# Kernel tuning notes

Measured on AMD Instinct MI355X. Metric: run time of the kernel, lower is better.

The kernel has to match this reference:

```python
import jax, jax.numpy as jnp
import numpy as np

HEADS = 4
CH = 64  # hidden_channels (per-head out channels)
N_INT = 50000
N_LANE = 400000
E_PO = 400000
E_ADJ = 200000


def setup_inputs() -> dict:
    key = jax.random.key(0)
    ks = iter(jax.random.split(key, 32))
    rn = lambda shape, s=0.1: jax.random.normal(next(ks), shape, dtype=jnp.float32) * s
    inp = {
        'x_int': rn((N_INT, 16), 1.0),
        'x_lane': rn((N_LANE, 12), 1.0),
        'h0': jnp.zeros((N_INT, CH), jnp.float32),
        'enc_int_W': rn((16, CH)), 'enc_int_b': jnp.zeros((CH,), jnp.float32),
        'enc_lane_W': rn((12, CH)), 'enc_lane_b': jnp.zeros((CH,), jnp.float32),
        'Wsrc_po': rn((CH, HEADS * CH)), 'Wdst_po': rn((CH, HEADS * CH)),
        'att_src_po': rn((HEADS, CH)), 'att_dst_po': rn((HEADS, CH)),
        'bias_po': jnp.zeros((HEADS * CH,), jnp.float32),
        'Wsrc_adj': rn((CH, HEADS * CH)), 'Wdst_adj': rn((CH, HEADS * CH)),
        'att_src_adj': rn((HEADS, CH)), 'att_dst_adj': rn((HEADS, CH)),
        'bias_adj': jnp.zeros((HEADS * CH,), jnp.float32),
        'gru_W_ih': rn((3 * CH, HEADS * CH)), 'gru_W_hh': rn((3 * CH, CH)),
        'gru_b_ih': jnp.zeros((3 * CH,), jnp.float32), 'gru_b_hh': jnp.zeros((3 * CH,), jnp.float32),
        'W_pi': rn((CH, 8)), 'b_pi': jnp.zeros((8,), jnp.float32),
        'W_v': rn((CH, 1)), 'b_v': jnp.zeros((1,), jnp.float32),
        'src_po': jax.random.randint(next(ks), (E_PO,), 0, N_LANE),
        'dst_po': jax.random.randint(next(ks), (E_PO,), 0, N_INT),
        'src_adj': jax.random.randint(next(ks), (E_ADJ,), 0, N_INT),
        'dst_adj': jax.random.randint(next(ks), (E_ADJ,), 0, N_INT),
    }
    return inp


def gat_conv(x_src, x_dst, src, dst, Wsrc, Wdst, a_src, a_dst, bias, n_dst):
    # PyG GATConv (bipartite, concat=True, no self loops), negative_slope=0.2
    hs = (x_src @ Wsrc).reshape(-1, HEADS, CH)  # [Ns,H,C]
    hd = (x_dst @ Wdst).reshape(-1, HEADS, CH)  # [Nd,H,C]
    a_s = jnp.einsum('nhc,hc->nh', hs, a_src)   # [Ns,H]
    a_d = jnp.einsum('nhc,hc->nh', hd, a_dst)   # [Nd,H]
    alpha = jax.nn.leaky_relu(a_s[src] + a_d[dst], 0.2)        # [E,H]
    amax = jax.ops.segment_max(alpha, dst, num_segments=n_dst)  # [Nd,H]
    ex = jnp.exp(alpha - amax[dst])
    den = jax.ops.segment_sum(ex, dst, num_segments=n_dst)
    w = ex / den[dst]                                           # [E,H] softmax per dst
    msg = hs[src] * w[:, :, None]                               # [E,H,C]
    out = jax.ops.segment_sum(msg, dst, num_segments=n_dst)     # [Nd,H,C]
    return out.reshape(n_dst, HEADS * CH) + bias


def gru_cell(x, h, W_ih, W_hh, b_ih, b_hh):
    gi = x @ W_ih.T + b_ih
    gh = h @ W_hh.T + b_hh
    i_r, i_z, i_n = jnp.split(gi, 3, axis=1)
    h_r, h_z, h_n = jnp.split(gh, 3, axis=1)
    r = jax.nn.sigmoid(i_r + h_r)
    z = jax.nn.sigmoid(i_z + h_z)
    n = jnp.tanh(i_n + r * h_n)
    return (1.0 - z) * n + z * h


def reference(x_int, x_lane, h0, enc_int_W, enc_int_b, enc_lane_W, enc_lane_b,
              Wsrc_po, Wdst_po, att_src_po, att_dst_po, bias_po,
              Wsrc_adj, Wdst_adj, att_src_adj, att_dst_adj, bias_adj,
              gru_W_ih, gru_W_hh, gru_b_ih, gru_b_hh,
              W_pi, b_pi, W_v, b_v,
              src_po, dst_po, src_adj, dst_adj):
    # per-type encoders + ReLU
    e_int = jax.nn.relu(x_int @ enc_int_W + enc_int_b)    # [N_int,CH]
    e_lane = jax.nn.relu(x_lane @ enc_lane_W + enc_lane_b)  # [N_lane,CH]
    # HeteroConv aggr='sum' over relations targeting 'intersection'
    o_po = gat_conv(e_lane, e_int, src_po, dst_po, Wsrc_po, Wdst_po,
                    att_src_po, att_dst_po, bias_po, N_INT)
    o_adj = gat_conv(e_int, e_int, src_adj, dst_adj, Wsrc_adj, Wdst_adj,
                     att_src_adj, att_dst_adj, bias_adj, N_INT)
    inter = jax.nn.relu(o_po + o_adj)  # dropout = identity (deterministic eval)
    h_new = gru_cell(inter, h0, gru_W_ih, gru_W_hh, gru_b_ih, gru_b_hh)
    logits = h_new @ W_pi + b_pi
    value = h_new @ W_v + b_v
    return logits, value, h_new
```

## Files before the change

kernel.cpp:

```cpp
#include <hip/hip_runtime.h>

#define NI 50000
#define NL 400000
#define EPO 400000
#define EADJ 200000

#define K1_ITER 8
#define K2_ITER 4
#define K1_ROWS (32*K1_ITER)
#define K2_ROWS (32*K2_ITER)
#define NLB ((NL + K1_ROWS - 1)/K1_ROWS)
#define NIB ((NI + K2_ROWS - 1)/K2_ROWS)
#define NHB ((EPO + EADJ + 255)/256)

typedef unsigned int u32;
typedef unsigned short u16;
typedef short bf16x8 __attribute__((ext_vector_type(8)));
typedef float f32x4 __attribute__((ext_vector_type(4)));

__device__ __forceinline__ float bf2f(u16 h){ return __uint_as_float(((u32)h)<<16); }
__device__ __forceinline__ u16 f2bf(float f){
  u32 u = __float_as_uint(f);
  u += 0x7FFFu + ((u>>16)&1u);
  return (u16)(u>>16);
}
__device__ __forceinline__ u32 pack2(float a, float b){
  return (u32)f2bf(a) | ((u32)f2bf(b)<<16);
}

__device__ __forceinline__ float b2_val(
    const float* __restrict__ W_ih, const float* __restrict__ W_hh, int m, int k)
{
  if(k < 256){ return (m<192) ? W_ih[m*256+k] : 0.f; }
  int kk = k-256;
  if(m<128) return W_hh[m*64+kk];
  if(m>=192) return W_hh[(m-64)*64+kk];
  return 0.f;
}

__global__ __launch_bounds__(256) void k0_prep(
    const float* __restrict__ Wsrc_po, const float* __restrict__ att_src_po,
    const float* __restrict__ Wdst_po, const float* __restrict__ att_dst_po,
    const float* __restrict__ Wsrc_adj, const float* __restrict__ att_src_adj,
    const float* __restrict__ Wdst_adj, const float* __restrict__ att_dst_adj,
    const float* __restrict__ W_ih, const float* __restrict__ W_hh,
    const float* __restrict__ bias_po, const float* __restrict__ bias_adj,
    const float* __restrict__ b_ih, const float* __restrict__ b_hh,
    float* __restrict__ v4, u16* __restrict__ WheadT, u16* __restrict__ B2F,
    float* __restrict__ bias_comb, float* __restrict__ bias2,
    int* __restrict__ cnt)
{
  const int T0 = 1024, T1 = 4*64*128, T2 = 10*16*64*8;
  const int TC = 2*NI;
  int total = T0 + T1 + T2 + 256 + 256 + TC;
  for(int t = blockIdx.x*256 + threadIdx.x; t < total; t += gridDim.x*256){
    if(t < T0){
      int which = t>>8, hc = t&255, h = hc>>6, c = hc&63;
      const float *W, *att;
      if(which==0){ W=Wsrc_po;  att=att_src_po; }
      else if(which==1){ W=Wdst_po;  att=att_dst_po; }
      else if(which==2){ W=Wsrc_adj; att=att_src_adj; }
      else { W=Wdst_adj; att=att_dst_adj; }
      float s=0.f;
      for(int j=0;j<64;j++) s += W[c*256 + h*64 + j]*att[h*64+j];
      v4[which*256 + hc] = s;
    } else if(t < T0 + T1){
      int i = t - T0; int h = i>>13, rem = i&8191, m = rem>>7, k = rem&127;
      float val = (k<64) ? Wsrc_po[k*256 + h*64 + m]
                         : Wsrc_adj[(k-64)*256 + h*64 + m];
      WheadT[i] = f2bf(val);
    } else if(t < T0 + T1 + T2){
      int i = t - (T0+T1);
      int j = i&7;
      int u4 = i>>3;
      int kstep = u4>>10, rem = u4&1023, tile = rem>>6, lane = rem&63;
      int col = tile*16 + (lane&15);
      int k = kstep*32 + (lane>>4)*8 + j;
      B2F[i] = f2bf(b2_val(W_ih, W_hh, col, k));
    } else if(t < T0 + T1 + T2 + 256){
      int m = t - (T0+T1+T2);
      bias_comb[m] = bias_po[m] + bias_adj[m];
    } else if(t < T0 + T1 + T2 + 512){
      int m = t - (T0+T1+T2+256);
      float v;
      if(m<128) v = b_ih[m] + b_hh[m];
      else if(m<192) v = b_ih[m];
      else v = b_hh[m-64];
      bias2[m] = v;
    } else {
      cnt[t - (T0+T1+T2+512)] = 0;
    }
  }
}

__global__ __launch_bounds__(256) void k_enc(
    const float* __restrict__ x_lane, const float* __restrict__ Wl, const float* __restrict__ bl,
    const float* __restrict__ x_int,  const float* __restrict__ Wi, const float* __restrict__ bi,
    const float* __restrict__ v_sp, const float* __restrict__ v_dp,
    const float* __restrict__ v_sa, const float* __restrict__ v_da,
    u16* __restrict__ e_lane, float* __restrict__ a_s_po,
    u16* __restrict__ e_int, float* __restrict__ a_dp, float* __restrict__ a_sa,
    float* __restrict__ a_da,
    const int* __restrict__ dst_po, const int* __restrict__ dst_adj,
    int* __restrict__ cnt)
{
  int t = threadIdx.x;
  int wv = t>>6, l = t&63;
  int g = l&7, m = l>>3;
  int blk = blockIdx.x;
  if(blk < NLB){
    float wreg[12][8], breg[8];
#pragma unroll
    for(int k=0;k<12;k++){
      float4 w0 = *(const float4*)(Wl + k*64 + g*8);
      float4 w1 = *(const float4*)(Wl + k*64 + g*8 + 4);
      wreg[k][0]=w0.x; wreg[k][1]=w0.y; wreg[k][2]=w0.z; wreg[k][3]=w0.w;
      wreg[k][4]=w1.x; wreg[k][5]=w1.y; wreg[k][6]=w1.z; wreg[k][7]=w1.w;
    }
    {
      float4 b0 = *(const float4*)(bl + g*8);
      float4 b1 = *(const float4*)(bl + g*8 + 4);
      breg[0]=b0.x; breg[1]=b0.y; breg[2]=b0.z; breg[3]=b0.w;
      breg[4]=b1.x; breg[5]=b1.y; breg[6]=b1.z; breg[7]=b1.w;
    }
    int rowbase = blk*K1_ROWS + wv*(8*K1_ITER) + m;
    float4 Aa={0,0,0,0}, Ab={0,0,0,0}, Ac={0,0,0,0};
    float4 Ba={0,0,0,0}, Bb={0,0,0,0}, Bc={0,0,0,0};
    if(rowbase < NL){
      const float4* xp = (const float4*)(x_lane + (size_t)rowbase*12);
      Aa = xp[0]; Ab = xp[1]; Ac = xp[2];
    }
    if(rowbase+8 < NL){
      const float4* xp = (const float4*)(x_lane + (size_t)(rowbase+8)*12);
      Ba = xp[0]; Bb = xp[1]; Bc = xp[2];
    }
#pragma unroll
    for(int it=0; it<K1_ITER; it++){
      int row = rowbase + it*8;
      float4 Ca={0,0,0,0}, Cb={0,0,0,0}, Cc={0,0,0,0};
      if(it+2 < K1_ITER && row+16 < NL){
        const float4* xp = (const float4*)(x_lane + (size_t)(row+16)*12);
        Ca = xp[0]; Cb = xp[1]; Cc = xp[2];
      }
      float xv[12];
      xv[0]=Aa.x; xv[1]=Aa.y; xv[2]=Aa.z; xv[3]=Aa.w;
      xv[4]=Ab.x; xv[5]=Ab.y; xv[6]=Ab.z; xv[7]=Ab.w;
      xv[8]=Ac.x; xv[9]=Ac.y; xv[10]=Ac.z; xv[11]=Ac.w;
      float acc[8];
#pragma unroll
      for(int j=0;j<8;j++) acc[j]=breg[j];
#pragma unroll
      for(int k=0;k<12;k++){
        float xk = xv[k];
#pragma unroll
        for(int j=0;j<8;j++) acc[j] += xk*wreg[k][j];
      }
      float e[8];
#pragma unroll
      for(int j=0;j<8;j++) e[j] = fmaxf(acc[j], 0.f);
      float as[4];
#pragma unroll
      for(int h=0;h<4;h++){
        float4 v0 = *(const float4*)(v_sp + h*64 + g*8);
        float4 v1 = *(const float4*)(v_sp + h*64 + g*8 + 4);
        as[h] = e[0]*v0.x + e[1]*v0.y + e[2]*v0.z + e[3]*v0.w
              + e[4]*v1.x + e[5]*v1.y + e[6]*v1.z + e[7]*v1.w;
      }
#pragma unroll
      for(int o=1;o<8;o<<=1){
#pragma unroll
        for(int h=0;h<4;h++) as[h] += __shfl_xor(as[h], o, 64);
      }
      if(row < NL){
        uint4 P;
        P.x = pack2(e[0],e[1]); P.y = pack2(e[2],e[3]);
        P.z = pack2(e[4],e[5]); P.w = pack2(e[6],e[7]);
        ((uint4*)e_lane)[(size_t)row*8 + g] = P;
        if(g==0){
          float4 A; A.x=as[0]; A.y=as[1]; A.z=as[2]; A.w=as[3];
          *(float4*)(a_s_po + (size_t)row*4) = A;
        }
      }
      Aa=Ba; Ab=Bb; Ac=Bc;
      Ba=Ca; Bb=Cb; Bc=Cc;
    }
  } else if(blk < NLB + NIB){
    int b2 = blk - NLB;
    float breg[8];
    {
      float4 b0 = *(const float4*)(bi + g*8);
      float4 b1 = *(const float4*)(bi + g*8 + 4);
      breg[0]=b0.x; breg[1]=b0.y; breg[2]=b0.z; breg[3]=b0.w;
      breg[4]=b1.x; breg[5]=b1.y; breg[6]=b1.z; breg[7]=b1.w;
    }
    int rowbase = b2*K2_ROWS + wv*(8*K2_ITER) + m;
#pragma unroll
    for(int it=0; it<K2_ITER; it++){
      int row = rowbase + it*8;
      float xv[16];
      if(row < NI){
        const float4* xp = (const float4*)(x_int + (size_t)row*16);
#pragma unroll
        for(int q=0;q<4;q++){
          float4 xq = xp[q];
          xv[q*4]=xq.x; xv[q*4+1]=xq.y; xv[q*4+2]=xq.z; xv[q*4+3]=xq.w;
        }
      } else {
#pragma unroll
        for(int k=0;k<16;k++) xv[k]=0.f;
      }
      float acc[8];
#pragma unroll
      for(int j=0;j<8;j++) acc[j]=breg[j];
#pragma unroll
      for(int k=0;k<16;k++){
        float4 w0 = *(const float4*)(Wi + k*64 + g*8);
        float4 w1 = *(const float4*)(Wi + k*64 + g*8 + 4);
        float xk = xv[k];
        acc[0] += xk*w0.x; acc[1] += xk*w0.y; acc[2] += xk*w0.z; acc[3] += xk*w0.w;
        acc[4] += xk*w1.x; acc[5] += xk*w1.y; acc[6] += xk*w1.z; acc[7] += xk*w1.w;
      }
      float e[8];
#pragma unroll
      for(int j=0;j<8;j++) e[j] = fmaxf(acc[j], 0.f);
      float ad[4], sa[4], da[4];
#pragma unroll
      for(int h=0;h<4;h++){
        float4 v0, v1;
        v0 = *(const float4*)(v_dp + h*64 + g*8); v1 = *(const float4*)(v_dp + h*64 + g*8 + 4);
        ad[h] = e[0]*v0.x + e[1]*v0.y + e[2]*v0.z + e[3]*v0.w
              + e[4]*v1.x + e[5]*v1.y + e[6]*v1.z + e[7]*v1.w;
        v0 = *(const float4*)(v_sa + h*64 + g*8); v1 = *(const float4*)(v_sa + h*64 + g*8 + 4);
        sa[h] = e[0]*v0.x + e[1]*v0.y + e[2]*v0.z + e[3]*v0.w
              + e[4]*v1.x + e[5]*v1.y + e[6]*v1.z + e[7]*v1.w;
        v0 = *(const float4*)(v_da + h*64 + g*8); v1 = *(const float4*)(v_da + h*64 + g*8 + 4);
        da[h] = e[0]*v0.x + e[1]*v0.y + e[2]*v0.z + e[3]*v0.w
              + e[4]*v1.x + e[5]*v1.y + e[6]*v1.z + e[7]*v1.w;
      }
#pragma unroll
      for(int o=1;o<8;o<<=1){
#pragma unroll
        for(int h=0;h<4;h++){
          ad[h] += __shfl_xor(ad[h], o, 64);
          sa[h] += __shfl_xor(sa[h], o, 64);
          da[h] += __shfl_xor(da[h], o, 64);
        }
      }
      if(row < NI){
        uint4 P;
        P.x = pack2(e[0],e[1]); P.y = pack2(e[2],e[3]);
        P.z = pack2(e[4],e[5]); P.w = pack2(e[6],e[7]);
        ((uint4*)e_int)[(size_t)row*8 + g] = P;
        if(g==0){
          float4 A;
          A.x=ad[0]; A.y=ad[1]; A.z=ad[2]; A.w=ad[3]; *(float4*)(a_dp + (size_t)row*4) = A;
          A.x=sa[0]; A.y=sa[1]; A.z=sa[2]; A.w=sa[3]; *(float4*)(a_sa + (size_t)row*4) = A;
          A.x=da[0]; A.y=da[1]; A.z=da[2]; A.w=da[3]; *(float4*)(a_da + (size_t)row*4) = A;
        }
      }
    }
  } else {
    int i = (blk - NLB - NIB)*256 + t;
    if(i < EPO) atomicAdd(&cnt[dst_po[i]], 1);
    else if(i < EPO+EADJ) atomicAdd(&cnt[NI + dst_adj[i-EPO]], 1);
  }
}

__global__ __launch_bounds__(1024) void k4a_scan(
    const int* __restrict__ cnt, int* __restrict__ offA, int* __restrict__ bsum)
{
  __shared__ int s[1024];
  int y = blockIdx.y;
  int i = blockIdx.x*1024 + threadIdx.x;
  int v = (i<NI) ? cnt[y*NI+i] : 0;
  s[threadIdx.x]=v;
  __syncthreads();
  for(int o=1;o<1024;o<<=1){
    int t = (threadIdx.x>=o) ? s[threadIdx.x-o] : 0;
    __syncthreads();
    s[threadIdx.x] += t;
    __syncthreads();
  }
  if(i<NI) offA[y*NI+i] = s[threadIdx.x]-v;
  if(threadIdx.x==1023) bsum[y*64+blockIdx.x] = s[1023];
}

__global__ __launch_bounds__(128) void k4b_scanb(int* __restrict__ bsum)
{
  int y = threadIdx.x>>6, lane = threadIdx.x&63;
  int v = (lane<49) ? bsum[y*64+lane] : 0;
  int orig = v;
#pragma unroll
  for(int o=1;o<64;o<<=1){
    int t = __shfl_up(v,o,64);
    if(lane>=o) v += t;
  }
  if(lane<49) bsum[y*64+lane] = v-orig;
}

__global__ __launch_bounds__(1024) void k4c_add(
    int* __restrict__ offA, int* __restrict__ cur, const int* __restrict__ bsum)
{
  int y = blockIdx.y;
  int i = blockIdx.x*1024 + threadIdx.x;
  if(i<NI){
    int o = offA[y*NI+i] + bsum[y*64+blockIdx.x];
    offA[y*NI+i]=o;
    cur[y*NI+i]=o;
  }
}

__global__ __launch_bounds__(256) void k5_scatter(
    const int* __restrict__ src_po, const int* __restrict__ dst_po,
    const int* __restrict__ src_adj, const int* __restrict__ dst_adj,
    const float* __restrict__ a_s_po, const float* __restrict__ a_d_po,
    const float* __restrict__ a_s_adj, const float* __restrict__ a_d_adj,
    int* __restrict__ cur, int* __restrict__ csr_po, int* __restrict__ csr_adj,
    float* __restrict__ pw_po, float* __restrict__ pw_adj)
{
  int i = blockIdx.x*256 + threadIdx.x;
  if(i < EPO){
    int s = src_po[i];
    int d = dst_po[i];
    int p = atomicAdd(&cur[d],1);
    csr_po[p] = s;
    float4 as = *(const float4*)(a_s_po + (size_t)s*4);
    float4 ad = *(const float4*)(a_d_po + (size_t)d*4);
    float4 pv;
    float x;
    x = as.x+ad.x; pv.x = __expf(x>0.f?x:0.2f*x);
    x = as.y+ad.y; pv.y = __expf(x>0.f?x:0.2f*x);
    x = as.z+ad.z; pv.z = __expf(x>0.f?x:0.2f*x);
    x = as.w+ad.w; pv.w = __expf(x>0.f?x:0.2f*x);
    *(float4*)(pw_po + (size_t)p*4) = pv;
  } else if(i < EPO+EADJ){
    int e = i-EPO;
    int s = src_adj[e];
    int d = dst_adj[e];
    int p = atomicAdd(&cur[NI+d],1);
    csr_adj[p] = s;
    float4 as = *(const float4*)(a_s_adj + (size_t)s*4);
    float4 ad = *(const float4*)(a_d_adj + (size_t)d*4);
    float4 pv;
    float x;
    x = as.x+ad.x; pv.x = __expf(x>0.f?x:0.2f*x);
    x = as.y+ad.y; pv.y = __expf(x>0.f?x:0.2f*x);
    x = as.z+ad.z; pv.z = __expf(x>0.f?x:0.2f*x);
    x = as.w+ad.w; pv.w = __expf(x>0.f?x:0.2f*x);
    *(float4*)(pw_adj + (size_t)p*4) = pv;
  }
}

__device__ __forceinline__ void agg_rel(
    int beg, int n, int lane,
    const int* __restrict__ csr, const float* __restrict__ pw,
    const u16* __restrict__ emat, u16* __restrict__ aggrow)
{
  float l0=0,l1=0,l2=0,l3=0;
  float c0=0,c1=0,c2=0,c3=0;
  for(int base=0;base<n;base+=64){
    int m = n-base; if(m>64) m=64;
    int sv_ = (lane<m) ? csr[beg+base+lane] : 0;
    int t2=0;
    for(; t2+1<m; t2+=2){
      int s0 = __shfl(sv_, t2, 64);
      int s1 = __shfl(sv_, t2+1, 64);
      float4 p0 = *(const float4*)(pw + (size_t)(beg+base+t2)*4);
      float4 p1 = *(const float4*)(pw + (size_t)(beg+base+t2+1)*4);
      float e0 = bf2f(emat[(size_t)s0*64+lane]);
      float e1 = bf2f(emat[(size_t)s1*64+lane]);
      c0 += p0.x*e0; c1 += p0.y*e0; c2 += p0.z*e0; c3 += p0.w*e0;
      l0 += p0.x;    l1 += p0.y;    l2 += p0.z;    l3 += p0.w;
      c0 += p1.x*e1; c1 += p1.y*e1; c2 += p1.z*e1; c3 += p1.w*e1;
      l0 += p1.x;    l1 += p1.y;    l2 += p1.z;    l3 += p1.w;
    }
    if(t2<m){
      int s0 = __shfl(sv_, t2, 64);
      float4 p0 = *(const float4*)(pw + (size_t)(beg+base+t2)*4);
      float e0 = bf2f(emat[(size_t)s0*64+lane]);
      c0 += p0.x*e0; c1 += p0.y*e0; c2 += p0.z*e0; c3 += p0.w*e0;
      l0 += p0.x;    l1 += p0.y;    l2 += p0.z;    l3 += p0.w;
    }
  }
  aggrow[lane]       = f2bf(n>0 ? c0/l0 : 0.f);
  aggrow[64+lane]    = f2bf(n>0 ? c1/l1 : 0.f);
  aggrow[128+lane]   = f2bf(n>0 ? c2/l2 : 0.f);
  aggrow[192+lane]   = f2bf(n>0 ? c3/l3 : 0.f);
}

__global__ __launch_bounds__(512) void k6_agg(
    const int* __restrict__ off, const int* __restrict__ cnt,
    const int* __restrict__ csr_po, const int* __restrict__ csr_adj,
    const float* __restrict__ pw_po, const float* __restrict__ pw_adj,
    const u16* __restrict__ e_lane, const u16* __restrict__ e_int,
    u16* __restrict__ agg)
{
  int wave=threadIdx.x>>6, lane=threadIdx.x&63;
  int d = blockIdx.x*4 + (wave&3);
  if(d>=NI) return;
  if(wave < 4)
    agg_rel(off[d],    cnt[d],    lane, csr_po,  pw_po,  e_lane, agg + (size_t)d*512);
  else
    agg_rel(off[NI+d], cnt[NI+d], lane, csr_adj, pw_adj, e_int,  agg + (size_t)d*512 + 256);
}

__global__ __launch_bounds__(256) void gemm_head(
    const u16* __restrict__ agg, const u16* __restrict__ WheadT,
    const float* __restrict__ bias, u16* __restrict__ inter256)
{
  __shared__ u16 As[64][136];
  __shared__ u16 Bs[64][136];
  int t=threadIdx.x, wave=t>>6, lane=t&63;
  int h = blockIdx.y;
  int row0 = blockIdx.x*64;
  int r = lane&15, q = lane>>4;
  const uint4* Bsrc = (const uint4*)(WheadT + (size_t)h*8192);
#pragma unroll
  for(int it=0; it<4; it++){
    int idx = it*256 + t;
    int brow = idx>>4, u4 = idx&15;
    *(uint4*)&Bs[brow][u4*8] = Bsrc[idx];
    int grow = row0 + brow;
    uint4 v = {0,0,0,0};
    if(grow < NI){
      int co = (u4<8) ? (h*64 + u4*8) : (256 + h*64 + (u4-8)*8);
      v = *(const uint4*)(agg + (size_t)grow*512 + co);
    }
    *(uint4*)&As[brow][u4*8] = v;
  }
  __syncthreads();
  f32x4 acc0={0,0,0,0}, acc1={0,0,0,0}, acc2={0,0,0,0}, acc3={0,0,0,0};
#pragma unroll
  for(int ks=0; ks<4; ks++){
    bf16x8 af = *(const bf16x8*)&As[wave*16 + r][q*8 + ks*32];
    bf16x8 b0 = *(const bf16x8*)&Bs[ 0 + r][q*8 + ks*32];
    bf16x8 b1 = *(const bf16x8*)&Bs[16 + r][q*8 + ks*32];
    bf16x8 b2 = *(const bf16x8*)&Bs[32 + r][q*8 + ks*32];
    bf16x8 b3 = *(const bf16x8*)&Bs[48 + r][q*8 + ks*32];
    acc0 = __builtin_amdgcn_mfma_f32_16x16x32_bf16(af,b0,acc0,0,0,0);
    acc1 = __builtin_amdgcn_mfma_f32_16x16x32_bf16(af,b1,acc1,0,0,0);
    acc2 = __builtin_amdgcn_mfma_f32_16x16x32_bf16(af,b2,acc2,0,0,0);
    acc3 = __builtin_amdgcn_mfma_f32_16x16x32_bf16(af,b3,acc3,0,0,0);
  }
  int crow_base = row0 + wave*16 + q*4;
#pragma unroll
  for(int t2=0;t2<4;t2++){
    f32x4 a = (t2==0)?acc0 : (t2==1)?acc1 : (t2==2)?acc2 : acc3;
    int col = h*64 + t2*16 + r;
    float bcol = bias[col];
#pragma unroll
    for(int rr=0;rr<4;rr++){
      int row = crow_base + rr;
      if(row < NI)
        inter256[(size_t)row*256 + col] = f2bf(fmaxf(a[rr]+bcol, 0.f));
    }
  }
}

__global__ __launch_bounds__(256) void k9_gru(
    const u16* __restrict__ inter256, const uint4* __restrict__ B2F,
    const float* __restrict__ bias2, const float* __restrict__ h0,
    const float* __restrict__ Wpi, const float* __restrict__ bpi,
    const float* __restrict__ Wv, const float* __restrict__ bvp,
    float* __restrict__ out)
{
  int t=threadIdx.x, w=t>>6, lane=t&63;
  int r = lane&15, q = lane>>4;
  int row0 = blockIdx.x*64;
  int arow = row0 + w*16 + r;
  int arc = arow < NI ? arow : NI-1;
  const u16* Aptr = inter256 + (size_t)arc*256 + q*8;
  const float* h0r = h0 + (size_t)arc*64 + q*8;
  f32x4 acc[16];
#pragma unroll
  for(int i=0;i<16;i++) acc[i] = (f32x4){0,0,0,0};
#pragma unroll
  for(int ks=0; ks<10; ks++){
    bf16x8 af;
    if(ks < 8){
      af = *(const bf16x8*)(Aptr + ks*32);
    } else {
      const float* hp = h0r + (ks-8)*32;
      float4 f0 = *(const float4*)(hp);
      float4 f1 = *(const float4*)(hp+4);
      uint4 P;
      P.x = pack2(f0.x,f0.y); P.y = pack2(f0.z,f0.w);
      P.z = pack2(f1.x,f1.y); P.w = pack2(f1.z,f1.w);
      *(uint4*)&af = P;
    }
    const uint4* bp = B2F + ks*1024 + lane;
#pragma unroll
    for(int tt=0;tt<16;tt++){
      uint4 bu = bp[tt*64];
      bf16x8 bf; *(uint4*)&bf = bu;
      acc[tt] = __builtin_amdgcn_mfma_f32_16x16x32_bf16(af, bf, acc[tt], 0,0,0);
    }
  }
  float pk[4][8];
  float pv[4];
#pragma unroll
  for(int rr=0;rr<4;rr++){
    pv[rr]=0.f;
#pragma unroll
    for(int j=0;j<8;j++) pk[rr][j]=0.f;
  }
  int rbase = row0 + w*16 + q*4;
#pragma unroll
  for(int t2=0;t2<4;t2++){
    int c = t2*16 + r;
    float b0 = bias2[c], b1 = bias2[64+c], b2 = bias2[128+c], b3 = bias2[192+c];
    float wp[8];
#pragma unroll
    for(int j=0;j<8;j++) wp[j] = Wpi[c*8+j];
    float wv = Wv[c];
#pragma unroll
    for(int rr=0;rr<4;rr++){
      int row = rbase + rr;
      float g0 = acc[t2][rr]    + b0;
      float g1 = acc[t2+4][rr]  + b1;
      float g2 = acc[t2+8][rr]  + b2;
      float g3 = acc[t2+12][rr] + b3;
      float h0v = (row < NI) ? h0[(size_t)row*64 + c] : 0.f;
      float rg = 1.f/(1.f+__expf(-g0));
      float zg = 1.f/(1.f+__expf(-g1));
      float e2 = __expf(2.f*(g2 + rg*g3));
      float ng = 1.f - 2.f/(e2+1.f);
      float h = (1.f-zg)*ng + zg*h0v;
      if(row < NI) out[450000 + (size_t)row*64 + c] = h;
#pragma unroll
      for(int j=0;j<8;j++) pk[rr][j] += h*wp[j];
      pv[rr] += h*wv;
    }
  }
#pragma unroll
  for(int o=1;o<16;o<<=1){
#pragma unroll
    for(int rr=0;rr<4;rr++){
#pragma unroll
      for(int j=0;j<8;j++) pk[rr][j] += __shfl_xor(pk[rr][j], o, 64);
      pv[rr] += __shfl_xor(pv[rr], o, 64);
    }
  }
  if(r==0){
#pragma unroll
    for(int rr=0;rr<4;rr++){
      int row = rbase + rr;
      if(row < NI){
#pragma unroll
        for(int j=0;j<8;j++) out[(size_t)row*8 + j] = pk[rr][j] + bpi[j];
        out[400000 + row] = pv[rr] + bvp[0];
      }
    }
  }
}

extern "C" void kernel_launch(void* const* d_in, const int* in_sizes, int n_in,
                              void* d_out, int out_size, void* d_ws, size_t ws_size,
                              hipStream_t stream) {
  const float* x_int      = (const float*)d_in[0];
  const float* x_lane     = (const float*)d_in[1];
  const float* h0         = (const float*)d_in[2];
  const float* enc_int_W  = (const float*)d_in[3];
  const float* enc_int_b  = (const float*)d_in[4];
  const float* enc_lane_W = (const float*)d_in[5];
  const float* enc_lane_b = (const float*)d_in[6];
  const float* Wsrc_po    = (const float*)d_in[7];
  const float* Wdst_po    = (const float*)d_in[8];
  const float* att_src_po = (const float*)d_in[9];
  const float* att_dst_po = (const float*)d_in[10];
  const float* bias_po    = (const float*)d_in[11];
  const float* Wsrc_adj   = (const float*)d_in[12];
  const float* Wdst_adj   = (const float*)d_in[13];
  const float* att_src_adj= (const float*)d_in[14];
  const float* att_dst_adj= (const float*)d_in[15];
  const float* bias_adj   = (const float*)d_in[16];
  const float* gru_W_ih   = (const float*)d_in[17];
  const float* gru_W_hh   = (const float*)d_in[18];
  const float* gru_b_ih   = (const float*)d_in[19];
  const float* gru_b_hh   = (const float*)d_in[20];
  const float* W_pi       = (const float*)d_in[21];
  const float* b_pi       = (const float*)d_in[22];
  const float* W_v        = (const float*)d_in[23];
  const float* b_v        = (const float*)d_in[24];
  const int* src_po  = (const int*)d_in[25];
  const int* dst_po  = (const int*)d_in[26];
  const int* src_adj = (const int*)d_in[27];
  const int* dst_adj = (const int*)d_in[28];
  float* out = (float*)d_out;

  char* w = (char*)d_ws;
  size_t ofs = 0;
  auto alloc = [&](size_t bytes)->char*{
    char* p = w + ofs;
    ofs = (ofs + bytes + 255) & ~(size_t)255;
    return p;
  };
  u16*  e_lane   = (u16*)alloc((size_t)NL*64*2);
  u16*  e_int    = (u16*)alloc((size_t)NI*64*2);
  float* a_s_po  = (float*)alloc((size_t)NL*4*4);
  float* a_d_po  = (float*)alloc((size_t)NI*4*4);
  float* a_s_adj = (float*)alloc((size_t)NI*4*4);
  float* a_d_adj = (float*)alloc((size_t)NI*4*4);
  int*  cnt      = (int*)alloc((size_t)2*NI*4);
  int*  offA     = (int*)alloc((size_t)2*NI*4);
  int*  cur      = (int*)alloc((size_t)2*NI*4);
  int*  csr_po   = (int*)alloc((size_t)EPO*4);
  int*  csr_adj  = (int*)alloc((size_t)EADJ*4);
  float* pw_po   = (float*)alloc((size_t)EPO*4*4);
  float* pw_adj  = (float*)alloc((size_t)EADJ*4*4);
  int*  bsum     = (int*)alloc(2*64*4);
  u16*  agg      = (u16*)alloc((size_t)NI*512*2);
  u16*  inter256 = (u16*)alloc((size_t)NI*256*2);
  u16*  WheadT   = (u16*)alloc(4*64*128*2);
  u16*  B2F      = (u16*)alloc(10*16*64*8*2);
  float* v4      = (float*)alloc(4*256*4);
  float* bias_comb = (float*)alloc(256*4);
  float* bias2   = (float*)alloc(256*4);
  (void)ws_size; (void)n_in; (void)in_sizes; (void)out_size;

  k0_prep<<<256, 256, 0, stream>>>(
      Wsrc_po, att_src_po, Wdst_po, att_dst_po,
      Wsrc_adj, att_src_adj, Wdst_adj, att_dst_adj,
      gru_W_ih, gru_W_hh, bias_po, bias_adj, gru_b_ih, gru_b_hh,
      v4, WheadT, B2F, bias_comb, bias2, cnt);
  k_enc<<<NLB+NIB+NHB, 256, 0, stream>>>(
      x_lane, enc_lane_W, enc_lane_b,
      x_int, enc_int_W, enc_int_b,
      v4 + 0, v4 + 256, v4 + 512, v4 + 768,
      e_lane, a_s_po, e_int, a_d_po, a_s_adj, a_d_adj,
      dst_po, dst_adj, cnt);
  k4a_scan<<<dim3(49,2), 1024, 0, stream>>>(cnt, offA, bsum);
  k4b_scanb<<<1, 128, 0, stream>>>(bsum);
  k4c_add<<<dim3(49,2), 1024, 0, stream>>>(offA, cur, bsum);
  k5_scatter<<<(EPO+EADJ+255)/256, 256, 0, stream>>>(src_po, dst_po, src_adj, dst_adj,
      a_s_po, a_d_po, a_s_adj, a_d_adj,
      cur, csr_po, csr_adj, pw_po, pw_adj);
  k6_agg<<<(NI+3)/4, 512, 0, stream>>>(offA, cnt, csr_po, csr_adj,
      pw_po, pw_adj, e_lane, e_int, agg);
  gemm_head<<<dim3((NI+63)/64, 4), 256, 0, stream>>>(agg, WheadT, bias_comb, inter256);
  k9_gru<<<(NI+63)/64, 256, 0, stream>>>(inter256, (const uint4*)B2F, bias2, h0,
      W_pi, b_pi, W_v, b_v, out);
}
```

Baseline: 371.8 us.

## Fuse head GEMM into GRU kernel and merge scan into single kernel

Replaces the three-kernel offset scan with one two-block kernel in which each block serially scans its whole 50000-entry relation in 1024-element chunks using wave shuffles. The per-head projection GEMM is folded into the GRU kernel: each block loops over the four heads, keeps the ReLU'd intermediate tile in shared memory and feeds it straight into the GRU MFMAs. This removes the 25.6 MB global intermediate round-trip and three kernel launches. The trade-offs are a serial scan on only two blocks and much more shared memory per GRU block, which lowers occupancy.

```diff
diff --git a/kernel.cpp b/kernel.cpp
--- a/kernel.cpp
+++ b/kernel.cpp
@@ -266,47 +266,43 @@
   }
 }
 
-__global__ __launch_bounds__(1024) void k4a_scan(
-    const int* __restrict__ cnt, int* __restrict__ offA, int* __restrict__ bsum)
-{
-  __shared__ int s[1024];
-  int y = blockIdx.y;
-  int i = blockIdx.x*1024 + threadIdx.x;
-  int v = (i<NI) ? cnt[y*NI+i] : 0;
-  s[threadIdx.x]=v;
-  __syncthreads();
-  for(int o=1;o<1024;o<<=1){
-    int t = (threadIdx.x>=o) ? s[threadIdx.x-o] : 0;
+__global__ __launch_bounds__(1024) void k4_scan(
+    const int* __restrict__ cnt, int* __restrict__ offA, int* __restrict__ cur)
+{
+  __shared__ int swsum[16];
+  int y = blockIdx.x;
+  int tid = threadIdx.x;
+  int wid = tid>>6, lane = tid&63;
+  int running = 0;
+  for(int c0=0; c0<NI; c0+=1024){
+    int i = c0 + tid;
+    int v = (i<NI) ? cnt[(size_t)y*NI+i] : 0;
+    int x = v;
+#pragma unroll
+    for(int o=1;o<64;o<<=1){
+      int tt = __shfl_up(x,o,64);
+      if(lane>=o) x += tt;
+    }
+    if(lane==63) swsum[wid] = x;
     __syncthreads();
-    s[threadIdx.x] += t;
+    if(tid<16){
+      int wv_ = swsum[tid];
+#pragma unroll
+      for(int o=1;o<16;o<<=1){
+        int tt = __shfl_up(wv_,o,64);
+        if(tid>=o) wv_ += tt;
+      }
+      swsum[tid] = wv_;
+    }
     __syncthreads();
-  }
-  if(i<NI) offA[y*NI+i] = s[threadIdx.x]-v;
-  if(threadIdx.x==1023) bsum[y*64+blockIdx.x] = s[1023];
-}
-
-__global__ __launch_bounds__(128) void k4b_scanb(int* __restrict__ bsum)
-{
-  int y = threadIdx.x>>6, lane = threadIdx.x&63;
-  int v = (lane<49) ? bsum[y*64+lane] : 0;
-  int orig = v;
-#pragma unroll
-  for(int o=1;o<64;o<<=1){
-    int t = __shfl_up(v,o,64);
-    if(lane>=o) v += t;
-  }
-  if(lane<49) bsum[y*64+lane] = v-orig;
-}
-
-__global__ __launch_bounds__(1024) void k4c_add(
-    int* __restrict__ offA, int* __restrict__ cur, const int* __restrict__ bsum)
-{
-  int y = blockIdx.y;
-  int i = blockIdx.x*1024 + threadIdx.x;
-  if(i<NI){
-    int o = offA[y*NI+i] + bsum[y*64+blockIdx.x];
-    offA[y*NI+i]=o;
-    cur[y*NI+i]=o;
+    int wofs = (wid>0) ? swsum[wid-1] : 0;
+    int excl = running + wofs + x - v;
+    if(i<NI){
+      offA[(size_t)y*NI+i] = excl;
+      cur[(size_t)y*NI+i]  = excl;
+    }
+    running += swsum[15];
+    __syncthreads();
   }
 }
 
@@ -404,72 +400,76 @@
     agg_rel(off[NI+d], cnt[NI+d], lane, csr_adj, pw_adj, e_int,  agg + (size_t)d*512 + 256);
 }
 
-__global__ __launch_bounds__(256) void gemm_head(
+__global__ __launch_bounds__(256) void k8_fused(
     const u16* __restrict__ agg, const u16* __restrict__ WheadT,
-    const float* __restrict__ bias, u16* __restrict__ inter256)
-{
-  __shared__ u16 As[64][136];
-  __shared__ u16 Bs[64][136];
-  int t=threadIdx.x, wave=t>>6, lane=t&63;
-  int h = blockIdx.y;
-  int row0 = blockIdx.x*64;
-  int r = lane&15, q = lane>>4;
-  const uint4* Bsrc = (const uint4*)(WheadT + (size_t)h*8192);
-#pragma unroll
-  for(int it=0; it<4; it++){
-    int idx = it*256 + t;
-    int brow = idx>>4, u4 = idx&15;
-    *(uint4*)&Bs[brow][u4*8] = Bsrc[idx];
-    int grow = row0 + brow;
-    uint4 v = {0,0,0,0};
-    if(grow < NI){
-      int co = (u4<8) ? (h*64 + u4*8) : (256 + h*64 + (u4-8)*8);
-      v = *(const uint4*)(agg + (size_t)grow*512 + co);
-    }
-    *(uint4*)&As[brow][u4*8] = v;
-  }
-  __syncthreads();
-  f32x4 acc0={0,0,0,0}, acc1={0,0,0,0}, acc2={0,0,0,0}, acc3={0,0,0,0};
-#pragma unroll
-  for(int ks=0; ks<4; ks++){
-    bf16x8 af = *(const bf16x8*)&As[wave*16 + r][q*8 + ks*32];
-    bf16x8 b0 = *(const bf16x8*)&Bs[ 0 + r][q*8 + ks*32];
-    bf16x8 b1 = *(const bf16x8*)&Bs[16 + r][q*8 + ks*32];
-    bf16x8 b2 = *(const bf16x8*)&Bs[32 + r][q*8 + ks*32];
-    bf16x8 b3 = *(const bf16x8*)&Bs[48 + r][q*8 + ks*32];
-    acc0 = __builtin_amdgcn_mfma_f32_16x16x32_bf16(af,b0,acc0,0,0,0);
-    acc1 = __builtin_amdgcn_mfma_f32_16x16x32_bf16(af,b1,acc1,0,0,0);
-    acc2 = __builtin_amdgcn_mfma_f32_16x16x32_bf16(af,b2,acc2,0,0,0);
-    acc3 = __builtin_amdgcn_mfma_f32_16x16x32_bf16(af,b3,acc3,0,0,0);
-  }
-  int crow_base = row0 + wave*16 + q*4;
-#pragma unroll
-  for(int t2=0;t2<4;t2++){
-    f32x4 a = (t2==0)?acc0 : (t2==1)?acc1 : (t2==2)?acc2 : acc3;
-    int col = h*64 + t2*16 + r;
-    float bcol = bias[col];
-#pragma unroll
-    for(int rr=0;rr<4;rr++){
-      int row = crow_base + rr;
-      if(row < NI)
-        inter256[(size_t)row*256 + col] = f2bf(fmaxf(a[rr]+bcol, 0.f));
-    }
-  }
-}
-
-__global__ __launch_bounds__(256) void k9_gru(
-    const u16* __restrict__ inter256, const uint4* __restrict__ B2F,
-    const float* __restrict__ bias2, const float* __restrict__ h0,
+    const float* __restrict__ bias_comb,
+    const uint4* __restrict__ B2F, const float* __restrict__ bias2,
+    const float* __restrict__ h0,
     const float* __restrict__ Wpi, const float* __restrict__ bpi,
     const float* __restrict__ Wv, const float* __restrict__ bvp,
     float* __restrict__ out)
 {
+  __shared__ u16 As[64][136];
+  __shared__ u16 Bs[64][136];
+  __shared__ u16 interT[64][264];
   int t=threadIdx.x, w=t>>6, lane=t&63;
   int r = lane&15, q = lane>>4;
   int row0 = blockIdx.x*64;
-  int arow = row0 + w*16 + r;
+
+  for(int h=0;h<4;h++){
+    const uint4* Bsrc = (const uint4*)(WheadT + (size_t)h*8192);
+    uint4 bvr[4], avr[4];
+#pragma unroll
+    for(int it=0; it<4; it++){
+      int idx = it*256 + t;
+      bvr[it] = Bsrc[idx];
+      int brow = idx>>4, u4 = idx&15;
+      int grow = row0 + brow;
+      uint4 v = {0,0,0,0};
+      if(grow < NI){
+        int co = (u4<8) ? (h*64 + u4*8) : (256 + h*64 + (u4-8)*8);
+        v = *(const uint4*)(agg + (size_t)grow*512 + co);
+      }
+      avr[it] = v;
+    }
+    __syncthreads();
+#pragma unroll
+    for(int it=0; it<4; it++){
+      int idx = it*256 + t;
+      int brow = idx>>4, u4 = idx&15;
+      *(uint4*)&Bs[brow][u4*8] = bvr[it];
+      *(uint4*)&As[brow][u4*8] = avr[it];
+    }
+    __syncthreads();
+    f32x4 acc0={0,0,0,0}, acc1={0,0,0,0}, acc2={0,0,0,0}, acc3={0,0,0,0};
+#pragma unroll
+    for(int ks=0; ks<4; ks++){
+      bf16x8 af = *(const bf16x8*)&As[w*16 + r][q*8 + ks*32];
+      bf16x8 b0 = *(const bf16x8*)&Bs[ 0 + r][q*8 + ks*32];
+      bf16x8 b1 = *(const bf16x8*)&Bs[16 + r][q*8 + ks*32];
+      bf16x8 b2 = *(const bf16x8*)&Bs[32 + r][q*8 + ks*32];
+      bf16x8 b3 = *(const bf16x8*)&Bs[48 + r][q*8 + ks*32];
+      acc0 = __builtin_amdgcn_mfma_f32_16x16x32_bf16(af,b0,acc0,0,0,0);
+      acc1 = __builtin_amdgcn_mfma_f32_16x16x32_bf16(af,b1,acc1,0,0,0);
+      acc2 = __builtin_amdgcn_mfma_f32_16x16x32_bf16(af,b2,acc2,0,0,0);
+      acc3 = __builtin_amdgcn_mfma_f32_16x16x32_bf16(af,b3,acc3,0,0,0);
+    }
+    int crow = w*16 + q*4;
+#pragma unroll
+    for(int t2=0;t2<4;t2++){
+      f32x4 a = (t2==0)?acc0 : (t2==1)?acc1 : (t2==2)?acc2 : acc3;
+      int col = h*64 + t2*16 + r;
+      float bcol = bias_comb[col];
+#pragma unroll
+      for(int rr=0;rr<4;rr++)
+        interT[crow+rr][col] = f2bf(fmaxf(a[rr]+bcol, 0.f));
+    }
+  }
+  __syncthreads();
+
+  int arowl = w*16 + r;
+  int arow  = row0 + arowl;
   int arc = arow < NI ? arow : NI-1;
-  const u16* Aptr = inter256 + (size_t)arc*256 + q*8;
   const float* h0r = h0 + (size_t)arc*64 + q*8;
   f32x4 acc[16];
 #pragma unroll
@@ -478,7 +478,7 @@
   for(int ks=0; ks<10; ks++){
     bf16x8 af;
     if(ks < 8){
-      af = *(const bf16x8*)(Aptr + ks*32);
+      af = *(const bf16x8*)&interT[arowl][ks*32 + q*8];
     } else {
       const float* hp = h0r + (ks-8)*32;
       float4 f0 = *(const float4*)(hp);
@@ -608,9 +608,7 @@
   int*  csr_adj  = (int*)alloc((size_t)EADJ*4);
   float* pw_po   = (float*)alloc((size_t)EPO*4*4);
   float* pw_adj  = (float*)alloc((size_t)EADJ*4*4);
-  int*  bsum     = (int*)alloc(2*64*4);
   u16*  agg      = (u16*)alloc((size_t)NI*512*2);
-  u16*  inter256 = (u16*)alloc((size_t)NI*256*2);
   u16*  WheadT   = (u16*)alloc(4*64*128*2);
   u16*  B2F      = (u16*)alloc(10*16*64*8*2);
   float* v4      = (float*)alloc(4*256*4);
@@ -629,15 +627,12 @@
       v4 + 0, v4 + 256, v4 + 512, v4 + 768,
       e_lane, a_s_po, e_int, a_d_po, a_s_adj, a_d_adj,
       dst_po, dst_adj, cnt);
-  k4a_scan<<<dim3(49,2), 1024, 0, stream>>>(cnt, offA, bsum);
-  k4b_scanb<<<1, 128, 0, stream>>>(bsum);
-  k4c_add<<<dim3(49,2), 1024, 0, stream>>>(offA, cur, bsum);
+  k4_scan<<<2, 1024, 0, stream>>>(cnt, offA, cur);
   k5_scatter<<<(EPO+EADJ+255)/256, 256, 0, stream>>>(src_po, dst_po, src_adj, dst_adj,
       a_s_po, a_d_po, a_s_adj, a_d_adj,
       cur, csr_po, csr_adj, pw_po, pw_adj);
   k6_agg<<<(NI+3)/4, 512, 0, stream>>>(offA, cnt, csr_po, csr_adj,
       pw_po, pw_adj, e_lane, e_int, agg);
-  gemm_head<<<dim3((NI+63)/64, 4), 256, 0, stream>>>(agg, WheadT, bias_comb, inter256);
-  k9_gru<<<(NI+63)/64, 256, 0, stream>>>(inter256, (const uint4*)B2F, bias2, h0,
-      W_pi, b_pi, W_v, b_v, out);
-}
+  k8_fused<<<(NI+63)/64, 256, 0, stream>>>(agg, WheadT, bias_comb,
+      (const uint4*)B2F, bias2, h0, W_pi, b_pi, W_v, b_v, out);
+}
```

New measurement: 401.9 us. 8.1% more time.

## Fuse head GEMM into GRU kernel via shared-memory intermediate

Applied to the files above, without the earlier changes.

Merges the per-head projection GEMM and the GRU/output kernel into a single kernel. The head outputs for a 64-row tile now go to a shared-memory buffer instead of the global inter256 array, which is removed. This drops one launch and a global write-then-read of a 25.6 MB intermediate. In exchange, each block loops over the four heads serially, with more shared memory per block and fewer blocks in flight, which may reduce parallelism in that stage.

```diff
diff --git a/kernel.cpp b/kernel.cpp
--- a/kernel.cpp
+++ b/kernel.cpp
@@ -404,72 +404,76 @@
     agg_rel(off[NI+d], cnt[NI+d], lane, csr_adj, pw_adj, e_int,  agg + (size_t)d*512 + 256);
 }
 
-__global__ __launch_bounds__(256) void gemm_head(
+__global__ __launch_bounds__(256) void k8_fused(
     const u16* __restrict__ agg, const u16* __restrict__ WheadT,
-    const float* __restrict__ bias, u16* __restrict__ inter256)
-{
-  __shared__ u16 As[64][136];
-  __shared__ u16 Bs[64][136];
-  int t=threadIdx.x, wave=t>>6, lane=t&63;
-  int h = blockIdx.y;
-  int row0 = blockIdx.x*64;
-  int r = lane&15, q = lane>>4;
-  const uint4* Bsrc = (const uint4*)(WheadT + (size_t)h*8192);
-#pragma unroll
-  for(int it=0; it<4; it++){
-    int idx = it*256 + t;
-    int brow = idx>>4, u4 = idx&15;
-    *(uint4*)&Bs[brow][u4*8] = Bsrc[idx];
-    int grow = row0 + brow;
-    uint4 v = {0,0,0,0};
-    if(grow < NI){
-      int co = (u4<8) ? (h*64 + u4*8) : (256 + h*64 + (u4-8)*8);
-      v = *(const uint4*)(agg + (size_t)grow*512 + co);
-    }
-    *(uint4*)&As[brow][u4*8] = v;
-  }
-  __syncthreads();
-  f32x4 acc0={0,0,0,0}, acc1={0,0,0,0}, acc2={0,0,0,0}, acc3={0,0,0,0};
-#pragma unroll
-  for(int ks=0; ks<4; ks++){
-    bf16x8 af = *(const bf16x8*)&As[wave*16 + r][q*8 + ks*32];
-    bf16x8 b0 = *(const bf16x8*)&Bs[ 0 + r][q*8 + ks*32];
-    bf16x8 b1 = *(const bf16x8*)&Bs[16 + r][q*8 + ks*32];
-    bf16x8 b2 = *(const bf16x8*)&Bs[32 + r][q*8 + ks*32];
-    bf16x8 b3 = *(const bf16x8*)&Bs[48 + r][q*8 + ks*32];
-    acc0 = __builtin_amdgcn_mfma_f32_16x16x32_bf16(af,b0,acc0,0,0,0);
-    acc1 = __builtin_amdgcn_mfma_f32_16x16x32_bf16(af,b1,acc1,0,0,0);
-    acc2 = __builtin_amdgcn_mfma_f32_16x16x32_bf16(af,b2,acc2,0,0,0);
-    acc3 = __builtin_amdgcn_mfma_f32_16x16x32_bf16(af,b3,acc3,0,0,0);
-  }
-  int crow_base = row0 + wave*16 + q*4;
-#pragma unroll
-  for(int t2=0;t2<4;t2++){
-    f32x4 a = (t2==0)?acc0 : (t2==1)?acc1 : (t2==2)?acc2 : acc3;
-    int col = h*64 + t2*16 + r;
-    float bcol = bias[col];
-#pragma unroll
-    for(int rr=0;rr<4;rr++){
-      int row = crow_base + rr;
-      if(row < NI)
-        inter256[(size_t)row*256 + col] = f2bf(fmaxf(a[rr]+bcol, 0.f));
-    }
-  }
-}
-
-__global__ __launch_bounds__(256) void k9_gru(
-    const u16* __restrict__ inter256, const uint4* __restrict__ B2F,
-    const float* __restrict__ bias2, const float* __restrict__ h0,
+    const float* __restrict__ bias_comb,
+    const uint4* __restrict__ B2F, const float* __restrict__ bias2,
+    const float* __restrict__ h0,
     const float* __restrict__ Wpi, const float* __restrict__ bpi,
     const float* __restrict__ Wv, const float* __restrict__ bvp,
     float* __restrict__ out)
 {
+  __shared__ u16 As[64][136];
+  __shared__ u16 Bs[64][136];
+  __shared__ u16 interT[64][264];
   int t=threadIdx.x, w=t>>6, lane=t&63;
   int r = lane&15, q = lane>>4;
   int row0 = blockIdx.x*64;
-  int arow = row0 + w*16 + r;
+
+  for(int h=0;h<4;h++){
+    const uint4* Bsrc = (const uint4*)(WheadT + (size_t)h*8192);
+    uint4 bvr[4], avr[4];
+#pragma unroll
+    for(int it=0; it<4; it++){
+      int idx = it*256 + t;
+      bvr[it] = Bsrc[idx];
+      int brow = idx>>4, u4 = idx&15;
+      int grow = row0 + brow;
+      uint4 v = {0,0,0,0};
+      if(grow < NI){
+        int co = (u4<8) ? (h*64 + u4*8) : (256 + h*64 + (u4-8)*8);
+        v = *(const uint4*)(agg + (size_t)grow*512 + co);
+      }
+      avr[it] = v;
+    }
+    __syncthreads();
+#pragma unroll
+    for(int it=0; it<4; it++){
+      int idx = it*256 + t;
+      int brow = idx>>4, u4 = idx&15;
+      *(uint4*)&Bs[brow][u4*8] = bvr[it];
+      *(uint4*)&As[brow][u4*8] = avr[it];
+    }
+    __syncthreads();
+    f32x4 acc0={0,0,0,0}, acc1={0,0,0,0}, acc2={0,0,0,0}, acc3={0,0,0,0};
+#pragma unroll
+    for(int ks=0; ks<4; ks++){
+      bf16x8 af = *(const bf16x8*)&As[w*16 + r][q*8 + ks*32];
+      bf16x8 b0 = *(const bf16x8*)&Bs[ 0 + r][q*8 + ks*32];
+      bf16x8 b1 = *(const bf16x8*)&Bs[16 + r][q*8 + ks*32];
+      bf16x8 b2 = *(const bf16x8*)&Bs[32 + r][q*8 + ks*32];
+      bf16x8 b3 = *(const bf16x8*)&Bs[48 + r][q*8 + ks*32];
+      acc0 = __builtin_amdgcn_mfma_f32_16x16x32_bf16(af,b0,acc0,0,0,0);
+      acc1 = __builtin_amdgcn_mfma_f32_16x16x32_bf16(af,b1,acc1,0,0,0);
+      acc2 = __builtin_amdgcn_mfma_f32_16x16x32_bf16(af,b2,acc2,0,0,0);
+      acc3 = __builtin_amdgcn_mfma_f32_16x16x32_bf16(af,b3,acc3,0,0,0);
+    }
+    int crow = w*16 + q*4;
+#pragma unroll
+    for(int t2=0;t2<4;t2++){
+      f32x4 a = (t2==0)?acc0 : (t2==1)?acc1 : (t2==2)?acc2 : acc3;
+      int col = h*64 + t2*16 + r;
+      float bcol = bias_comb[col];
+#pragma unroll
+      for(int rr=0;rr<4;rr++)
+        interT[crow+rr][col] = f2bf(fmaxf(a[rr]+bcol, 0.f));
+    }
+  }
+  __syncthreads();
+
+  int arowl = w*16 + r;
+  int arow  = row0 + arowl;
   int arc = arow < NI ? arow : NI-1;
-  const u16* Aptr = inter256 + (size_t)arc*256 + q*8;
   const float* h0r = h0 + (size_t)arc*64 + q*8;
   f32x4 acc[16];
 #pragma unroll
@@ -478,7 +482,7 @@
   for(int ks=0; ks<10; ks++){
     bf16x8 af;
     if(ks < 8){
-      af = *(const bf16x8*)(Aptr + ks*32);
+      af = *(const bf16x8*)&interT[arowl][ks*32 + q*8];
     } else {
       const float* hp = h0r + (ks-8)*32;
       float4 f0 = *(const float4*)(hp);
@@ -610,7 +614,6 @@
   float* pw_adj  = (float*)alloc((size_t)EADJ*4*4);
   int*  bsum     = (int*)alloc(2*64*4);
   u16*  agg      = (u16*)alloc((size_t)NI*512*2);
-  u16*  inter256 = (u16*)alloc((size_t)NI*256*2);
   u16*  WheadT   = (u16*)alloc(4*64*128*2);
   u16*  B2F      = (u16*)alloc(10*16*64*8*2);
   float* v4      = (float*)alloc(4*256*4);
@@ -637,7 +640,6 @@
       cur, csr_po, csr_adj, pw_po, pw_adj);
   k6_agg<<<(NI+3)/4, 512, 0, stream>>>(offA, cnt, csr_po, csr_adj,
       pw_po, pw_adj, e_lane, e_int, agg);
-  gemm_head<<<dim3((NI+63)/64, 4), 256, 0, stream>>>(agg, WheadT, bias_comb, inter256);
-  k9_gru<<<(NI+63)/64, 256, 0, stream>>>(inter256, (const uint4*)B2F, bias2, h0,
-      W_pi, b_pi, W_v, b_v, out);
-}
+  k8_fused<<<(NI+63)/64, 256, 0, stream>>>(agg, WheadT, bias_comb,
+      (const uint4*)B2F, bias2, h0, W_pi, b_pi, W_v, b_v, out);
+}
```

After: 369.7 us. No clear change (-0.6%).
